# Optimization experiments

Measured on AMD Instinct MI355X. Metric: run time of the kernel, lower is better.

The kernel has to match this reference:

```python
import jax, jax.numpy as jnp
import numpy as np

B, V, T = 512, 50257, 2048   # batch, vocab, history length
TOP_K = 50                    # from __init__ arg top_k
NEG_INF = jnp.float32(-1e30)  # finite stand-in for -inf (same softmax result, clean grads)


def setup_inputs() -> dict:
    key = jax.random.key(0)
    k1, k2, k3 = jax.random.split(key, 3)
    logits = jax.random.normal(k1, (B, V), jnp.float32) * 4.0
    previous_tokens = jax.random.randint(k2, (B, T), 0, V)
    # uniform noise for the Gumbel-max trick (torch.rand_like); avoid log(0)
    rand_u = jax.random.uniform(k3, (B, V), jnp.float32, minval=1e-10, maxval=1.0)
    return {
        "logits": logits,
        "previous_tokens": previous_tokens,
        "rand_u": rand_u,
        "temperature": jnp.full((1, 1), 0.8, jnp.float32),
        "top_p": jnp.full((1, 1), 0.8, jnp.float32),
        "repetition_penalty": jnp.full((1, 1), 1.35, jnp.float32),
    }


def _logits_to_probs(logits, previous_tokens, temperature, top_p, repetition_penalty):
    b = jnp.arange(logits.shape[0])[:, None]
    # repetition penalty: gather scores at previous tokens, rescale, scatter back
    score = jnp.take_along_axis(logits, previous_tokens, axis=1)            # [B, T]
    score = jnp.where(score < 0, score * repetition_penalty, score / repetition_penalty)
    logits = logits.at[b, previous_tokens].set(score)
    # top-p (nucleus) filtering: sort descending, cumulative softmax mass
    order = jnp.argsort(-logits, axis=-1)                                   # [B, V]
    sorted_logits = jnp.take_along_axis(logits, order, axis=1)
    cum_probs = jnp.cumsum(jax.nn.softmax(sorted_logits, axis=-1), axis=-1)
    remove_sorted = cum_probs > top_p
    remove_sorted = remove_sorted.at[:, 0].set(False)                       # always keep best token
    # unsort the removal mask back to vocab order (order is a permutation)
    remove = jnp.zeros_like(remove_sorted).at[b, order].set(remove_sorted)
    logits = jnp.where(remove, NEG_INF, logits)
    # temperature
    logits = logits / jnp.maximum(temperature, 1e-5)
    # top-k filtering: mask everything below the k-th largest logit
    v = jax.lax.top_k(logits, TOP_K)[0]                                     # [B, TOP_K]
    pivot = v[:, -1:]
    logits = jnp.where(logits < pivot, NEG_INF, logits)
    return jax.nn.softmax(logits, axis=-1)


def reference(logits, previous_tokens, rand_u, temperature, top_p, repetition_penalty):
    probs = _logits_to_probs(logits, previous_tokens, temperature, top_p, repetition_penalty)
    # Gumbel-max multinomial sample: argmax(probs / Exp(1))
    q = -jnp.log(rand_u)
    idx_next = jnp.argmax(probs / q, axis=-1, keepdims=True).astype(jnp.int64)
    return idx_next, probs
```

## Files before the change

### kernel.cpp

```cpp
#include <hip/hip_runtime.h>
#include <cstdint>
#include <cmath>

#define V_SIZE 50257
#define T_SIZE 2048
#define B_SIZE 512
#define CAND_MAX 1024
#define SPEC_THRESH 10.0f
#define SPEC_MIN 80
#define KOFF 32.0f

#define NTHR 1024
#define NWAVE (NTHR / 64)

#define BM_WORDS ((V_SIZE + 31) / 32)

extern "C" __global__ __launch_bounds__(NTHR, 8)
void fused_kernel(const float* __restrict__ logits,
                  const int*   __restrict__ prev,
                  const float* __restrict__ rand_u,
                  const float* __restrict__ tempp,
                  const float* __restrict__ toppp,
                  const float* __restrict__ repp,
                  float* __restrict__ out)
{
    const int row  = blockIdx.x;
    const int tid  = threadIdx.x;
    const int lane = tid & 63;
    const int wid  = tid >> 6;

    __shared__ unsigned int bitmap[BM_WORDS];
    __shared__ float cval[CAND_MAX];
    __shared__ int   cidx[CAND_MAX];
    __shared__ float rbuf[CAND_MAX];
    __shared__ float redf[NWAVE];
    __shared__ float redm[NWAVE];
    __shared__ int   redi[NWAVE];
    __shared__ float sM, sZ, sS, sStot;
    __shared__ int   sCnt, sSend;

    const float rp   = repp[0];
    const float topp = toppp[0];
    const float temp = fmaxf(tempp[0], 1e-5f);

    const size_t rowoff = (size_t)row * V_SIZE;
    const float* lrow = logits + rowoff;
    const float* urow = rand_u + rowoff;
    float*       orow = out + B_SIZE + rowoff;

    for (int i = tid; i < BM_WORDS; i += NTHR) bitmap[i] = 0u;
    if (tid == 0) sCnt = 0;
    __syncthreads();

    const int head  = (4 - (row & 3)) & 3;
    const int nvec  = (V_SIZE - head) >> 2;
    const int tails = head + nvec * 4;
    const float4* lrow4 = (const float4*)(lrow + head);

    float lz0 = 0.0f, lz1 = 0.0f;
    auto collect = [&](float x, int v) {
        if (x > SPEC_THRESH) {
            int p = atomicAdd(&sCnt, 1);
            if (p < CAND_MAX) { cval[p] = x; cidx[p] = v; }
        }
    };
    if (tid < head) {
        float x = lrow[tid];
        collect(x, tid);
        lz0 += __expf(x - KOFF);
    }
    if (tid < V_SIZE - tails) {
        float x = lrow[tails + tid];
        collect(x, tails + tid);
        lz0 += __expf(x - KOFF);
    }
    for (int i = tid; i < nvec; i += NTHR) {
        float4 x4 = lrow4[i];
        int v = head + i * 4;
        collect(x4.x, v);     collect(x4.y, v + 1);
        collect(x4.z, v + 2); collect(x4.w, v + 3);
        lz0 += __expf(x4.x - KOFF) + __expf(x4.z - KOFF);
        lz1 += __expf(x4.y - KOFF) + __expf(x4.w - KOFF);
    }

    const int* prow = prev + (size_t)row * T_SIZE;
    float corr = 0.0f;
    for (int i = tid; i < T_SIZE; i += NTHR) {
        int v = prow[i];
        unsigned bit = 1u << (v & 31);
        unsigned old = atomicOr(&bitmap[((unsigned)v) >> 5], bit);
        if (!(old & bit)) {
            float x  = lrow[v];
            float xp = (x < 0.0f) ? x * rp : x / rp;
            corr += __expf(xp - KOFF) - __expf(x - KOFF);
        }
    }
    __syncthreads();

    const int Craw = sCnt;
    int C = min(Craw, CAND_MAX);
    for (int i = tid; i < C; i += NTHR) {
        int v = cidx[i];
        if ((bitmap[((unsigned)v) >> 5] >> (v & 31)) & 1u) {
            float x = cval[i];
            cval[i] = (x < 0.0f) ? x * rp : x / rp;
        }
    }
    {
        float wz = lz0 + lz1 + corr;
        for (int off = 32; off; off >>= 1) wz += __shfl_down(wz, off);
        if (lane == 0) redf[wid] = wz;
    }
    __syncthreads();

    {
        float lm = -INFINITY;
        for (int i = tid; i < C; i += NTHR) lm = fmaxf(lm, cval[i]);
        for (int off = 32; off; off >>= 1) lm = fmaxf(lm, __shfl_down(lm, off));
        if (lane == 0) redm[wid] = lm;
    }
    __syncthreads();
    if (tid == 0) {
        float s = 0.0f, m = -INFINITY;
        for (int i = 0; i < NWAVE; ++i) { s += redf[i]; m = fmaxf(m, redm[i]); }
        sStot = s; sM = m;
    }
    __syncthreads();

    float M = sM;
    float Z = sStot * expf(KOFF - M);
    bool ok = (Craw >= SPEC_MIN && Craw <= CAND_MAX && M > SPEC_THRESH);

    if (!ok) {
        float lm = -INFINITY, lz = 0.0f;
        for (int v = tid; v < V_SIZE; v += NTHR) {
            float x = lrow[v];
            if ((bitmap[((unsigned)v) >> 5] >> (v & 31)) & 1u)
                x = (x < 0.0f) ? x * rp : x / rp;
            lm = fmaxf(lm, x);
            lz += __expf(x - KOFF);
        }
        {
            float wm = lm;
            for (int off = 32; off; off >>= 1) wm = fmaxf(wm, __shfl_down(wm, off));
            if (lane == 0) redm[wid] = wm;
        }
        __syncthreads();
        if (tid == 0) {
            float m = redm[0];
            for (int i = 1; i < NWAVE; ++i) m = fmaxf(m, redm[i]);
            sM = m;
        }
        __syncthreads();
        M = sM;
        {
            float wz = lz;
            for (int off = 32; off; off >>= 1) wz += __shfl_down(wz, off);
            if (lane == 0) redf[wid] = wz;
        }
        __syncthreads();
        if (tid == 0) {
            float s = 0.0f;
            for (int i = 0; i < NWAVE; ++i) s += redf[i];
            sZ = s * expf(KOFF - M);
        }
        __syncthreads();
        Z = sZ;

        auto count_pass = [&](float thr) -> int {
            __syncthreads();
            if (tid == 0) sCnt = 0;
            __syncthreads();
            int local = 0;
            for (int v = tid; v < V_SIZE; v += NTHR) {
                float x = lrow[v];
                if ((bitmap[((unsigned)v) >> 5] >> (v & 31)) & 1u)
                    x = (x < 0.0f) ? x * rp : x / rp;
                if (x > thr) local++;
            }
            if (local) atomicAdd(&sCnt, local);
            __syncthreads();
            return sCnt;
        };
        float a = -200.0f, b = 200.0f, thr = 0.0f;
        int c = 0;
        for (int it = 0; it < 40; ++it) {
            thr = 0.5f * (a + b);
            c = count_pass(thr);
            if (c < SPEC_MIN)       b = thr;
            else if (c > CAND_MAX)  a = thr;
            else break;
        }
        if (c < SPEC_MIN) thr = a;
        __syncthreads();
        if (tid == 0) sCnt = 0;
        __syncthreads();
        for (int v = tid; v < V_SIZE; v += NTHR) {
            float x = lrow[v];
            if ((bitmap[((unsigned)v) >> 5] >> (v & 31)) & 1u)
                x = (x < 0.0f) ? x * rp : x / rp;
            if (x > thr) {
                int p = atomicAdd(&sCnt, 1);
                if (p < CAND_MAX) { cval[p] = x; cidx[p] = v; }
            }
        }
        __syncthreads();
        C = min(sCnt, CAND_MAX);
    }

    int n = 1; while (n < C) n <<= 1;
    for (int i = C + tid; i < n; i += NTHR) { cval[i] = -INFINITY; cidx[i] = 0x7FFFFFFF; }
    __syncthreads();

    if (n <= 512) {
        const int t = tid;
        const bool act = (t < n);
        float v = 0.0f; int id = 0;
        if (act) { v = cval[t]; id = cidx[t]; }
        for (int k = 2; k <= n; k <<= 1) {
            for (int j = k >> 1; j > 0; j >>= 1) {
                float pv = 0.0f; int pid = 0;
                if (j >= 64) {
                    __syncthreads();
                    if (act) { cval[t] = v; cidx[t] = id; }
                    __syncthreads();
                    if (act) { pv = cval[t ^ j]; pid = cidx[t ^ j]; }
                } else if (act) {
                    pv  = __shfl_xor(v, j);
                    pid = __shfl_xor(id, j);
                }
                if (act) {
                    const bool amLow = ((t & j) == 0);
                    const float vi = amLow ? v : pv,  vl = amLow ? pv : v;
                    const int   ii = amLow ? id : pid, il = amLow ? pid : id;
                    const bool lFirst = (vl > vi) || (vl == vi && il < ii);
                    const bool asc = ((t & k) == 0);
                    if (lFirst == asc) { v = pv; id = pid; }
                }
            }
        }
        __syncthreads();
        if (act) { cval[t] = v; cidx[t] = id; }
        __syncthreads();
    } else {
        for (int k = 2; k <= n; k <<= 1) {
            for (int j = k >> 1; j > 0; j >>= 1) {
                for (int i = tid; i < n; i += NTHR) {
                    int l = i ^ j;
                    if (l > i) {
                        float vi = cval[i], vl = cval[l];
                        int   ii = cidx[i], il = cidx[l];
                        bool lFirst = (vl > vi) || (vl == vi && il < ii);
                        bool asc = ((i & k) == 0);
                        if (lFirst == asc) {
                            cval[i] = vl; cval[l] = vi;
                            cidx[i] = il; cidx[l] = ii;
                        }
                    }
                }
                __syncthreads();
            }
        }
    }

    for (int i = tid; i < C; i += NTHR)
        rbuf[i] = expf(cval[i] - M) / Z;
    __syncthreads();

    if (tid == 0) {
        float cum = 0.0f;
        int m = 0;
        float vp = cval[min(49, C - 1)];
        for (int i = 0; i < C; ++i) {
            cum += rbuf[i];
            if (i > 0 && cum > topp) break;
            m = i;
            if (m >= 49 && cval[i] < vp) break;
        }
        int send;
        if (m >= 49) {
            int e = 49;
            while (e + 1 < C && cval[e + 1] == vp) ++e;
            send = (m < e) ? m : e;
        } else {
            send = m;
        }
        sSend = send;
    }
    __syncthreads();

    const int send = sSend;
    const float v0 = cval[0];
    for (int i = tid; i <= send; i += NTHR)
        rbuf[i] = expf(cval[i] / temp - v0 / temp);
    __syncthreads();
    if (tid == 0) {
        float S = 0.0f;
        for (int i = 0; i <= send; ++i) S += rbuf[i];
        sS = S;
    }
    __syncthreads();
    const float S = sS;

    float bestr = -1.0f;
    int   besti = 0x7FFFFFFF;
    for (int i = tid; i <= send; i += NTHR) {
        float p = rbuf[i] / S;
        int v = cidx[i];
        orow[v] = p;
        float q = -logf(urow[v]);
        float r = p / q;
        if (r > bestr || (r == bestr && v < besti)) { bestr = r; besti = v; }
    }
    for (int off = 32; off; off >>= 1) {
        float r2 = __shfl_down(bestr, off);
        int   i2 = __shfl_down(besti, off);
        if (r2 > bestr || (r2 == bestr && i2 < besti)) { bestr = r2; besti = i2; }
    }
    if (lane == 0) { redf[wid] = bestr; redi[wid] = besti; }
    __syncthreads();
    if (tid == 0) {
        float br = redf[0]; int bi = redi[0];
        for (int i = 1; i < NWAVE; ++i) {
            if (redf[i] > br || (redf[i] == br && redi[i] < bi)) { br = redf[i]; bi = redi[i]; }
        }
        out[row] = (float)bi;
    }
}

extern "C" void kernel_launch(void* const* d_in, const int* in_sizes, int n_in,
                              void* d_out, int out_size, void* d_ws, size_t ws_size,
                              hipStream_t stream) {
    const float* logits = (const float*)d_in[0];
    const int*   prev   = (const int*)d_in[1];
    const float* rand_u = (const float*)d_in[2];
    const float* tempp  = (const float*)d_in[3];
    const float* toppp  = (const float*)d_in[4];
    const float* repp   = (const float*)d_in[5];
    float* out = (float*)d_out;

    (void)hipMemsetAsync(d_out, 0, (size_t)out_size, stream);

    hipLaunchKernelGGL(fused_kernel, dim3(B_SIZE), dim3(NTHR), 0, stream,
                       logits, prev, rand_u, tempp, toppp, repp, out);
}
```

Measured before the change: 257.9 us.

## Build repetition bitmap first and apply penalty inline during the streaming pass

The previous-token bitmap is now built before the main pass over the logits row, so the penalty is applied inline while streaming. This removes the scattered re-gather of logits at previous tokens and the separate correction of exp-sums and candidate values. The main float4 loop is also unrolled 4x to keep more loads in flight, and two reductions are merged under one barrier. In exchange it adds an extra barrier and a 64-bit bitmap word read per float4, and the candidate set is now chosen after the penalty is applied rather than before.

```diff
diff --git a/kernel.cpp b/kernel.cpp
--- a/kernel.cpp
+++ b/kernel.cpp
@@ -29,7 +29,7 @@
     const int lane = tid & 63;
     const int wid  = tid >> 6;
 
-    __shared__ unsigned int bitmap[BM_WORDS];
+    __shared__ unsigned int bitmap[BM_WORDS + 1];
     __shared__ float cval[CAND_MAX];
     __shared__ int   cidx[CAND_MAX];
     __shared__ float rbuf[CAND_MAX];
@@ -48,8 +48,15 @@
     const float* urow = rand_u + rowoff;
     float*       orow = out + B_SIZE + rowoff;
 
-    for (int i = tid; i < BM_WORDS; i += NTHR) bitmap[i] = 0u;
+    for (int i = tid; i < BM_WORDS + 1; i += NTHR) bitmap[i] = 0u;
     if (tid == 0) sCnt = 0;
+    __syncthreads();
+
+    const int* prow = prev + (size_t)row * T_SIZE;
+    for (int i = tid; i < T_SIZE; i += NTHR) {
+        int v = prow[i];
+        atomicOr(&bitmap[((unsigned)v) >> 5], 1u << (v & 31));
+    }
     __syncthreads();
 
     const int head  = (4 - (row & 3)) & 3;
@@ -58,71 +65,67 @@
     const float4* lrow4 = (const float4*)(lrow + head);
 
     float lz0 = 0.0f, lz1 = 0.0f;
+    auto pen = [&](float x) { return (x < 0.0f) ? x * rp : x / rp; };
     auto collect = [&](float x, int v) {
         if (x > SPEC_THRESH) {
             int p = atomicAdd(&sCnt, 1);
             if (p < CAND_MAX) { cval[p] = x; cidx[p] = v; }
         }
     };
-    if (tid < head) {
-        float x = lrow[tid];
-        collect(x, tid);
+    auto proc1 = [&](float x, int v) {
+        unsigned w = bitmap[((unsigned)v) >> 5];
+        if ((w >> (v & 31)) & 1u) x = pen(x);
+        collect(x, v);
         lz0 += __expf(x - KOFF);
-    }
-    if (tid < V_SIZE - tails) {
-        float x = lrow[tails + tid];
-        collect(x, tails + tid);
-        lz0 += __expf(x - KOFF);
-    }
-    for (int i = tid; i < nvec; i += NTHR) {
-        float4 x4 = lrow4[i];
-        int v = head + i * 4;
-        collect(x4.x, v);     collect(x4.y, v + 1);
-        collect(x4.z, v + 2); collect(x4.w, v + 3);
-        lz0 += __expf(x4.x - KOFF) + __expf(x4.z - KOFF);
-        lz1 += __expf(x4.y - KOFF) + __expf(x4.w - KOFF);
-    }
-
-    const int* prow = prev + (size_t)row * T_SIZE;
-    float corr = 0.0f;
-    for (int i = tid; i < T_SIZE; i += NTHR) {
-        int v = prow[i];
-        unsigned bit = 1u << (v & 31);
-        unsigned old = atomicOr(&bitmap[((unsigned)v) >> 5], bit);
-        if (!(old & bit)) {
-            float x  = lrow[v];
-            float xp = (x < 0.0f) ? x * rp : x / rp;
-            corr += __expf(xp - KOFF) - __expf(x - KOFF);
-        }
-    }
+    };
+    auto proc4 = [&](float4 x4, int v) {
+        const int wi = ((unsigned)v) >> 5;
+        const unsigned sh = (unsigned)v & 31u;
+        unsigned long long w64 =
+            ((unsigned long long)bitmap[wi + 1] << 32) | (unsigned long long)bitmap[wi];
+        unsigned w = (unsigned)(w64 >> sh);
+        float a = x4.x, b = x4.y, c = x4.z, d = x4.w;
+        if (w & 1u) a = pen(a);
+        if (w & 2u) b = pen(b);
+        if (w & 4u) c = pen(c);
+        if (w & 8u) d = pen(d);
+        collect(a, v); collect(b, v + 1); collect(c, v + 2); collect(d, v + 3);
+        lz0 += __expf(a - KOFF) + __expf(c - KOFF);
+        lz1 += __expf(b - KOFF) + __expf(d - KOFF);
+    };
+
+    if (tid < head)           proc1(lrow[tid], tid);
+    if (tid < V_SIZE - tails) proc1(lrow[tails + tid], tails + tid);
+
+    int i = tid;
+    for (; i + 3 * NTHR < nvec; i += 4 * NTHR) {
+        float4 a0 = lrow4[i];
+        float4 a1 = lrow4[i + NTHR];
+        float4 a2 = lrow4[i + 2 * NTHR];
+        float4 a3 = lrow4[i + 3 * NTHR];
+        proc4(a0, head + i * 4);
+        proc4(a1, head + (i + NTHR) * 4);
+        proc4(a2, head + (i + 2 * NTHR) * 4);
+        proc4(a3, head + (i + 3 * NTHR) * 4);
+    }
+    for (; i < nvec; i += NTHR) proc4(lrow4[i], head + i * 4);
+
     __syncthreads();
 
     const int Craw = sCnt;
     int C = min(Craw, CAND_MAX);
-    for (int i = tid; i < C; i += NTHR) {
-        int v = cidx[i];
-        if ((bitmap[((unsigned)v) >> 5] >> (v & 31)) & 1u) {
-            float x = cval[i];
-            cval[i] = (x < 0.0f) ? x * rp : x / rp;
-        }
-    }
     {
-        float wz = lz0 + lz1 + corr;
+        float wz = lz0 + lz1;
         for (int off = 32; off; off >>= 1) wz += __shfl_down(wz, off);
-        if (lane == 0) redf[wid] = wz;
-    }
-    __syncthreads();
-
-    {
         float lm = -INFINITY;
-        for (int i = tid; i < C; i += NTHR) lm = fmaxf(lm, cval[i]);
+        for (int k = tid; k < C; k += NTHR) lm = fmaxf(lm, cval[k]);
         for (int off = 32; off; off >>= 1) lm = fmaxf(lm, __shfl_down(lm, off));
-        if (lane == 0) redm[wid] = lm;
+        if (lane == 0) { redf[wid] = wz; redm[wid] = lm; }
     }
     __syncthreads();
     if (tid == 0) {
         float s = 0.0f, m = -INFINITY;
-        for (int i = 0; i < NWAVE; ++i) { s += redf[i]; m = fmaxf(m, redm[i]); }
+        for (int k = 0; k < NWAVE; ++k) { s += redf[k]; m = fmaxf(m, redm[k]); }
         sStot = s; sM = m;
     }
     __syncthreads();
@@ -135,8 +138,7 @@
         float lm = -INFINITY, lz = 0.0f;
         for (int v = tid; v < V_SIZE; v += NTHR) {
             float x = lrow[v];
-            if ((bitmap[((unsigned)v) >> 5] >> (v & 31)) & 1u)
-                x = (x < 0.0f) ? x * rp : x / rp;
+            if ((bitmap[((unsigned)v) >> 5] >> (v & 31)) & 1u) x = pen(x);
             lm = fmaxf(lm, x);
             lz += __expf(x - KOFF);
         }
@@ -148,7 +150,7 @@
         __syncthreads();
         if (tid == 0) {
             float m = redm[0];
-            for (int i = 1; i < NWAVE; ++i) m = fmaxf(m, redm[i]);
+            for (int k = 1; k < NWAVE; ++k) m = fmaxf(m, redm[k]);
             sM = m;
         }
         __syncthreads();
@@ -161,7 +163,7 @@
         __syncthreads();
         if (tid == 0) {
             float s = 0.0f;
-            for (int i = 0; i < NWAVE; ++i) s += redf[i];
+            for (int k = 0; k < NWAVE; ++k) s += redf[k];
             sZ = s * expf(KOFF - M);
         }
         __syncthreads();
@@ -174,8 +176,7 @@
             int local = 0;
             for (int v = tid; v < V_SIZE; v += NTHR) {
                 float x = lrow[v];
-                if ((bitmap[((unsigned)v) >> 5] >> (v & 31)) & 1u)
-                    x = (x < 0.0f) ? x * rp : x / rp;
+                if ((bitmap[((unsigned)v) >> 5] >> (v & 31)) & 1u) x = pen(x);
                 if (x > thr) local++;
             }
             if (local) atomicAdd(&sCnt, local);
@@ -197,8 +198,7 @@
         __syncthreads();
         for (int v = tid; v < V_SIZE; v += NTHR) {
             float x = lrow[v];
-            if ((bitmap[((unsigned)v) >> 5] >> (v & 31)) & 1u)
-                x = (x < 0.0f) ? x * rp : x / rp;
+            if ((bitmap[((unsigned)v) >> 5] >> (v & 31)) & 1u) x = pen(x);
             if (x > thr) {
                 int p = atomicAdd(&sCnt, 1);
                 if (p < CAND_MAX) { cval[p] = x; cidx[p] = v; }
@@ -209,7 +209,7 @@
     }
 
     int n = 1; while (n < C) n <<= 1;
-    for (int i = C + tid; i < n; i += NTHR) { cval[i] = -INFINITY; cidx[i] = 0x7FFFFFFF; }
+    for (int k = C + tid; k < n; k += NTHR) { cval[k] = -INFINITY; cidx[k] = 0x7FFFFFFF; }
     __syncthreads();
 
     if (n <= 512) {
@@ -245,16 +245,16 @@
     } else {
         for (int k = 2; k <= n; k <<= 1) {
             for (int j = k >> 1; j > 0; j >>= 1) {
-                for (int i = tid; i < n; i += NTHR) {
-                    int l = i ^ j;
-                    if (l > i) {
-                        float vi = cval[i], vl = cval[l];
-                        int   ii = cidx[i], il = cidx[l];
+                for (int q = tid; q < n; q += NTHR) {
+                    int l = q ^ j;
+                    if (l > q) {
+                        float vi = cval[q], vl = cval[l];
+                        int   ii = cidx[q], il = cidx[l];
                         bool lFirst = (vl > vi) || (vl == vi && il < ii);
-                        bool asc = ((i & k) == 0);
+                        bool asc = ((q & k) == 0);
                         if (lFirst == asc) {
-                            cval[i] = vl; cval[l] = vi;
-                            cidx[i] = il; cidx[l] = ii;
+                            cval[q] = vl; cval[l] = vi;
+                            cidx[q] = il; cidx[l] = ii;
                         }
                     }
                 }
@@ -263,19 +263,19 @@
         }
     }
 
-    for (int i = tid; i < C; i += NTHR)
-        rbuf[i] = expf(cval[i] - M) / Z;
+    for (int k = tid; k < C; k += NTHR)
+        rbuf[k] = expf(cval[k] - M) / Z;
     __syncthreads();
 
     if (tid == 0) {
         float cum = 0.0f;
         int m = 0;
         float vp = cval[min(49, C - 1)];
-        for (int i = 0; i < C; ++i) {
-            cum += rbuf[i];
-            if (i > 0 && cum > topp) break;
-            m = i;
-            if (m >= 49 && cval[i] < vp) break;
+        for (int k = 0; k < C; ++k) {
+            cum += rbuf[k];
+            if (k > 0 && cum > topp) break;
+            m = k;
+            if (m >= 49 && cval[k] < vp) break;
         }
         int send;
         if (m >= 49) {
@@ -291,12 +291,12 @@
 
     const int send = sSend;
     const float v0 = cval[0];
-    for (int i = tid; i <= send; i += NTHR)
-        rbuf[i] = expf(cval[i] / temp - v0 / temp);
+    for (int k = tid; k <= send; k += NTHR)
+        rbuf[k] = expf(cval[k] / temp - v0 / temp);
     __syncthreads();
     if (tid == 0) {
         float S = 0.0f;
-        for (int i = 0; i <= send; ++i) S += rbuf[i];
+        for (int k = 0; k <= send; ++k) S += rbuf[k];
         sS = S;
     }
     __syncthreads();
@@ -304,9 +304,9 @@
 
     float bestr = -1.0f;
     int   besti = 0x7FFFFFFF;
-    for (int i = tid; i <= send; i += NTHR) {
-        float p = rbuf[i] / S;
-        int v = cidx[i];
+    for (int k = tid; k <= send; k += NTHR) {
+        float p = rbuf[k] / S;
+        int v = cidx[k];
         orow[v] = p;
         float q = -logf(urow[v]);
         float r = p / q;
@@ -321,8 +321,8 @@
     __syncthreads();
     if (tid == 0) {
         float br = redf[0]; int bi = redi[0];
-        for (int i = 1; i < NWAVE; ++i) {
-            if (redf[i] > br || (redf[i] == br && redi[i] < bi)) { br = redf[i]; bi = redi[i]; }
+        for (int k = 1; k < NWAVE; ++k) {
+            if (redf[k] > br || (redf[k] == br && redi[k] < bi)) { br = redf[k]; bi = redi[k]; }
         }
         out[row] = (float)bi;
     }
```

After: 246.5 us. 4.4% less time.
